# Performance work log

Hardware: AMD Instinct MI355X
Metric: run time of the kernel (lower is better)

Reference implementation:

```python
import jax, jax.numpy as jnp
import numpy as np


def setup_inputs() -> dict:
    key = jax.random.key(0)
    k_x, k_w1, k_w2 = jax.random.split(key, 3)
    B, N, F, H = 32, 1024, 512, 2048
    x = jax.random.normal(k_x, (B, N, F), dtype=jnp.float32)
    # first: orthogonal-ish init (Gaussian is fine as a stand-in for correctness testing)
    W1 = jax.random.normal(k_w1, (H, F), dtype=jnp.float32) / np.sqrt(F)
    b1 = jnp.zeros((H,), dtype=jnp.float32)
    # second: normal(std=0.01)
    W2 = jax.random.normal(k_w2, (F, H), dtype=jnp.float32) * 0.01
    b2 = jnp.zeros((F,), dtype=jnp.float32)
    return {"x": x, "W1": W1, "b1": b1, "W2": W2, "b2": b2, "dim": 1}


def reference(x, W1, b1, W2, b2, dim):
    # Move the target feature axis (1 + dim) to last position.
    x = jnp.moveaxis(x, 1 + dim, -1)  # [B, N, F]
    srt = jnp.argsort(x, axis=-1)     # argsort indices
    inv = jnp.argsort(srt, axis=-1)   # inverse permutation
    # torch: x.scatter(-1, argsort, x) -> out[argsort[i]] = x[i] == gather by inverse
    xs = jnp.take_along_axis(x, inv, axis=-1)
    # 2-layer MLP with skip
    h = jax.nn.relu(jnp.einsum('bnf,hf->bnh', xs, W1) + b1)
    y = jnp.einsum('bnh,fh->bnf', h, W2) + b2 + xs
    # torch: y.scatter(-1, inverse, y) -> out[inverse[i]] = y[i] == gather by argsort
    out = jnp.take_along_axis(y, srt, axis=-1)
    return jnp.moveaxis(out, -1, 1 + dim)
```

## Files before the change

### kernel.cpp

```cpp
#include <hip/hip_runtime.h>
#include <hip/hip_bf16.h>

typedef __hip_bfloat16 bf16;
typedef __attribute__((ext_vector_type(8))) short bf16x8;
typedef __attribute__((ext_vector_type(4))) float f32x4;

#define ASYNC_CP16(gsrc, ldst)                                                              \
  __builtin_amdgcn_global_load_lds(                                                         \
      (const __attribute__((address_space(1))) unsigned int*)(gsrc),                        \
      (__attribute__((address_space(3))) unsigned int*)(ldst), 16, 0, 0)

#define BB 32
#define NN 1024
#define FF 512
#define HH 2048
#define M_ROWS (BB * NN)

__global__ __launch_bounds__(256) void cvt_f32_bf16(const float* __restrict__ s,
                                                    bf16* __restrict__ d, int n) {
  int i = blockIdx.x * 256 + threadIdx.x;
  if (i < n) d[i] = __float2bfloat16(s[i]);
}

__global__ __launch_bounds__(256) void sort_rows_wave(const float* __restrict__ x,
                                                      unsigned* __restrict__ xs_pack,
                                                      unsigned* __restrict__ srt_pack) {
  __shared__ __align__(16) unsigned short scatx[4 * FF];
  const int t = threadIdx.x;
  const int lane = t & 63;
  const int w = t >> 6;
  const size_t row = (size_t)blockIdx.x * 4 + w;
  const float* xr = x + row * FF;

  float4 v0 = *(const float4*)(xr + lane * 8);
  float4 v1 = *(const float4*)(xr + lane * 8 + 4);
  float vals[8] = {v0.x, v0.y, v0.z, v0.w, v1.x, v1.y, v1.z, v1.w};

  unsigned long long key[8];
#pragma unroll
  for (int r = 0; r < 8; r++) {
    unsigned u = __float_as_uint(vals[r]);
    unsigned s = u ^ ((unsigned)((int)u >> 31) | 0x80000000u);
    key[r] = ((unsigned long long)s << 32) | (unsigned)(lane * 8 + r);
  }

#pragma unroll
  for (int k = 2; k <= 512; k <<= 1) {
#pragma unroll
    for (int j = k >> 1; j > 0; j >>= 1) {
      if (j >= 8) {
        const int d = j >> 3;
#pragma unroll
        for (int r = 0; r < 8; r++) {
          unsigned long long o = __shfl_xor(key[r], d, 64);
          bool asc = (((lane * 8 + r) & k) == 0);
          bool lower = ((lane & d) == 0);
          bool keepmin = (asc == lower);
          bool minemin = key[r] < o;
          key[r] = (minemin == keepmin) ? key[r] : o;
        }
      } else {
#pragma unroll
        for (int r = 0; r < 8; r++) {
          if ((r & j) == 0) {
            const int a = r, b = r | j;
            bool asc = (((lane * 8 + a) & k) == 0);
            unsigned long long ka = key[a], kb = key[b];
            bool sw = ((ka > kb) == asc);
            key[a] = sw ? kb : ka;
            key[b] = sw ? ka : kb;
          }
        }
      }
    }
  }

  const int base = w * FF;
  unsigned j8[8];
#pragma unroll
  for (int r = 0; r < 8; r++) {
    j8[r] = (unsigned)key[r] & 0xFFFFu;
    __hip_bfloat16 hb = __float2bfloat16(vals[r]);
    scatx[base + j8[r]] = *(unsigned short*)&hb;
  }

  uint4 so;
  so.x = j8[0] | (j8[1] << 16);
  so.y = j8[2] | (j8[3] << 16);
  so.z = j8[4] | (j8[5] << 16);
  so.w = j8[6] | (j8[7] << 16);
  *(uint4*)(srt_pack + row * 256 + lane * 4) = so;

  __syncthreads();
  uint4 xo = *(const uint4*)&scatx[base + lane * 8];
  *(uint4*)(xs_pack + row * 256 + lane * 4) = xo;
}

template <int RELU, int K, int N>
__global__ __launch_bounds__(512, 4) void gemm_fat(const bf16* __restrict__ A,
                                                   const bf16* __restrict__ Bw,
                                                   const float* __restrict__ bias,
                                                   bf16* __restrict__ C) {
  __shared__ __align__(16) bf16 As[128 * 32];
  __shared__ __align__(16) bf16 Bs[256 * 32];
  const int t = threadIdx.x;
  const int lane = t & 63, wave = t >> 6;
  const int waveM = wave >> 2, waveN = wave & 3;
  const int srow = lane >> 2;
  const int scol = (lane & 3) * 8;
  const size_t mBase = (size_t)blockIdx.x * 128;
  const size_t nBase = (size_t)blockIdx.y * 256;
  const bf16* Ag  = A  + (mBase + wave * 16 + srow) * (size_t)K + scol;
  const bf16* Bg0 = Bw + (nBase + wave * 32 + srow) * (size_t)K + scol;
  const bf16* Bg1 = Bw + (nBase + wave * 32 + 16 + srow) * (size_t)K + scol;
  bf16* Al  = &As[wave * 16 * 32];
  bf16* Bl0 = &Bs[wave * 32 * 32];
  bf16* Bl1 = &Bs[(wave * 32 + 16) * 32];
  const int fr = lane & 15;
  const int fk = (lane >> 4) * 8;

  f32x4 acc[4][4];
  f32x4 zero = {0.f, 0.f, 0.f, 0.f};
#pragma unroll
  for (int i = 0; i < 4; i++)
#pragma unroll
    for (int j = 0; j < 4; j++) acc[i][j] = zero;

  for (int k0 = 0; k0 < K; k0 += 32) {
    ASYNC_CP16(Ag + k0, Al);
    ASYNC_CP16(Bg0 + k0, Bl0);
    ASYNC_CP16(Bg1 + k0, Bl1);
    __syncthreads();
    bf16x8 af[4], bfr[4];
#pragma unroll
    for (int mt = 0; mt < 4; mt++)
      af[mt] = *(const bf16x8*)&As[(waveM * 64 + mt * 16 + fr) * 32 + fk];
#pragma unroll
    for (int nt = 0; nt < 4; nt++)
      bfr[nt] = *(const bf16x8*)&Bs[(waveN * 64 + nt * 16 + fr) * 32 + fk];
#pragma unroll
    for (int mt = 0; mt < 4; mt++)
#pragma unroll
      for (int nt = 0; nt < 4; nt++)
        acc[mt][nt] = __builtin_amdgcn_mfma_f32_16x16x32_bf16(af[mt], bfr[nt], acc[mt][nt], 0, 0, 0);
    __syncthreads();
  }

  const int cn = lane & 15;
  const int cm = (lane >> 4) * 4;
  float b4[4];
#pragma unroll
  for (int nt = 0; nt < 4; nt++) b4[nt] = bias[nBase + waveN * 64 + nt * 16 + cn];
#pragma unroll
  for (int mt = 0; mt < 4; mt++) {
#pragma unroll
    for (int nt = 0; nt < 4; nt++) {
      size_t gn = nBase + waveN * 64 + nt * 16 + cn;
#pragma unroll
      for (int r = 0; r < 4; r++) {
        size_t gm = mBase + waveM * 64 + mt * 16 + cm + r;
        float v = acc[mt][nt][r] + b4[nt];
        if (RELU) v = fmaxf(v, 0.f);
        C[gm * N + gn] = __float2bfloat16(v);
      }
    }
  }
}

__global__ __launch_bounds__(256) void permute_add(const bf16* __restrict__ z,
                                                   const unsigned* __restrict__ srt_pack,
                                                   const float* __restrict__ x,
                                                   float* __restrict__ out) {
  __shared__ __align__(16) unsigned short zr[4][FF];
  const int t = threadIdx.x;
  const int lane = t & 63;
  const int w = t >> 6;
  const size_t row = (size_t)blockIdx.x * 4 + w;

  *(uint4*)&zr[w][lane * 8] = *(const uint4*)(z + row * FF + lane * 8);
  uint4 sv = *(const uint4*)(srt_pack + row * 256 + lane * 4);
  float4 x0 = *(const float4*)(x + row * FF + lane * 8);
  float4 x1 = *(const float4*)(x + row * FF + lane * 8 + 4);
  __syncthreads();

  unsigned idx[8] = {sv.x & 0xFFFFu, sv.x >> 16, sv.y & 0xFFFFu, sv.y >> 16,
                     sv.z & 0xFFFFu, sv.z >> 16, sv.w & 0xFFFFu, sv.w >> 16};
  float xv[8] = {x0.x, x0.y, x0.z, x0.w, x1.x, x1.y, x1.z, x1.w};
  float4 o0, o1;
  float* op = &o0.x;
#pragma unroll
  for (int r = 0; r < 8; r++) {
    float zf = __uint_as_float(((unsigned)zr[w][idx[r]]) << 16);
    ((r < 4) ? (&o0.x) : (&o1.x))[r & 3] = zf + xv[r];
  }
  (void)op;
  *(float4*)(out + row * FF + lane * 8) = o0;
  *(float4*)(out + row * FF + lane * 8 + 4) = o1;
}

extern "C" void kernel_launch(void* const* d_in, const int* in_sizes, int n_in,
                              void* d_out, int out_size, void* d_ws, size_t ws_size,
                              hipStream_t stream) {
  const float* x  = (const float*)d_in[0];
  const float* W1 = (const float*)d_in[1];
  const float* b1 = (const float*)d_in[2];
  const float* W2 = (const float*)d_in[3];
  const float* b2 = (const float*)d_in[4];
  float* out = (float*)d_out;

  char* ws = (char*)d_ws;
  unsigned* xs  = (unsigned*)(ws);
  bf16*     z   = (bf16*)(ws);
  unsigned* srt = (unsigned*)(ws + 33554432);
  bf16* h   = (bf16*)(ws + 67108864);
  bf16* W1b = (bf16*)(ws + 201326592);
  bf16* W2b = (bf16*)(ws + 203423744);

  cvt_f32_bf16<<<(HH * FF + 255) / 256, 256, 0, stream>>>(W1, W1b, HH * FF);
  cvt_f32_bf16<<<(FF * HH + 255) / 256, 256, 0, stream>>>(W2, W2b, FF * HH);
  sort_rows_wave<<<M_ROWS / 4, 256, 0, stream>>>(x, xs, srt);
  gemm_fat<1, FF, HH><<<dim3(M_ROWS / 128, HH / 256), 512, 0, stream>>>((const bf16*)xs, W1b, b1, h);
  gemm_fat<0, HH, FF><<<dim3(M_ROWS / 128, FF / 256), 512, 0, stream>>>(h, W2b, b2, z);
  permute_add<<<M_ROWS / 4, 256, 0, stream>>>(z, srt, x, out);
}
```

Measured before the change: 414.1 us.

## Fuse skip add into second GEMM epilogue, use DPP in sort, merge weight casts

The residual add of the sorted input moves into the second GEMM's epilogue, which reads the bf16 sorted activations. The final permute kernel becomes a pure gather and no longer reads the fp32 input. The bitonic sort replaces some cross-lane shuffles (xor 1, 2, 8) with DPP moves, and the two weight-conversion kernels become one launch. In exchange, the skip term is now bf16-rounded rather than exact fp32, and the epilogue does extra strided bf16 loads.

```diff
diff --git a/kernel.cpp b/kernel.cpp
--- a/kernel.cpp
+++ b/kernel.cpp
@@ -16,10 +16,23 @@
 #define HH 2048
 #define M_ROWS (BB * NN)
 
-__global__ __launch_bounds__(256) void cvt_f32_bf16(const float* __restrict__ s,
-                                                    bf16* __restrict__ d, int n) {
+__global__ __launch_bounds__(256) void cvt_pair(const float* __restrict__ a, bf16* __restrict__ da,
+                                                const float* __restrict__ b, bf16* __restrict__ db,
+                                                int n) {
   int i = blockIdx.x * 256 + threadIdx.x;
-  if (i < n) d[i] = __float2bfloat16(s[i]);
+  if (i < n) {
+    da[i] = __float2bfloat16(a[i]);
+    db[i] = __float2bfloat16(b[i]);
+  }
+}
+
+template <int CTRL>
+__device__ __forceinline__ unsigned long long dpp_xor64(unsigned long long k) {
+  int lo = (int)(unsigned)k;
+  int hi = (int)(unsigned)(k >> 32);
+  int plo = __builtin_amdgcn_update_dpp(lo, lo, CTRL, 0xF, 0xF, false);
+  int phi = __builtin_amdgcn_update_dpp(hi, hi, CTRL, 0xF, 0xF, false);
+  return (((unsigned long long)(unsigned)phi) << 32) | (unsigned)plo;
 }
 
 __global__ __launch_bounds__(256) void sort_rows_wave(const float* __restrict__ x,
@@ -52,7 +65,11 @@
         const int d = j >> 3;
 #pragma unroll
         for (int r = 0; r < 8; r++) {
-          unsigned long long o = __shfl_xor(key[r], d, 64);
+          unsigned long long o;
+          if (d == 1)       o = dpp_xor64<0xB1>(key[r]);
+          else if (d == 2)  o = dpp_xor64<0x4E>(key[r]);
+          else if (d == 8)  o = dpp_xor64<0x128>(key[r]);
+          else              o = __shfl_xor(key[r], d, 64);
           bool asc = (((lane * 8 + r) & k) == 0);
           bool lower = ((lane & d) == 0);
           bool keepmin = (asc == lower);
@@ -96,10 +113,11 @@
   *(uint4*)(xs_pack + row * 256 + lane * 4) = xo;
 }
 
-template <int RELU, int K, int N>
+template <int RELU, int ADDX, int K, int N>
 __global__ __launch_bounds__(512, 4) void gemm_fat(const bf16* __restrict__ A,
                                                    const bf16* __restrict__ Bw,
                                                    const float* __restrict__ bias,
+                                                   const bf16* __restrict__ xs_add,
                                                    bf16* __restrict__ C) {
   __shared__ __align__(16) bf16 As[128 * 32];
   __shared__ __align__(16) bf16 Bs[256 * 32];
@@ -161,39 +179,34 @@
         size_t gm = mBase + waveM * 64 + mt * 16 + cm + r;
         float v = acc[mt][nt][r] + b4[nt];
         if (RELU) v = fmaxf(v, 0.f);
+        if (ADDX) v += __bfloat162float(xs_add[gm * N + gn]);
         C[gm * N + gn] = __float2bfloat16(v);
       }
     }
   }
 }
 
-__global__ __launch_bounds__(256) void permute_add(const bf16* __restrict__ z,
-                                                   const unsigned* __restrict__ srt_pack,
-                                                   const float* __restrict__ x,
-                                                   float* __restrict__ out) {
+__global__ __launch_bounds__(256) void permute_gather(const bf16* __restrict__ zp,
+                                                      const unsigned* __restrict__ srt_pack,
+                                                      float* __restrict__ out) {
   __shared__ __align__(16) unsigned short zr[4][FF];
   const int t = threadIdx.x;
   const int lane = t & 63;
   const int w = t >> 6;
   const size_t row = (size_t)blockIdx.x * 4 + w;
 
-  *(uint4*)&zr[w][lane * 8] = *(const uint4*)(z + row * FF + lane * 8);
+  *(uint4*)&zr[w][lane * 8] = *(const uint4*)(zp + row * FF + lane * 8);
   uint4 sv = *(const uint4*)(srt_pack + row * 256 + lane * 4);
-  float4 x0 = *(const float4*)(x + row * FF + lane * 8);
-  float4 x1 = *(const float4*)(x + row * FF + lane * 8 + 4);
   __syncthreads();
 
   unsigned idx[8] = {sv.x & 0xFFFFu, sv.x >> 16, sv.y & 0xFFFFu, sv.y >> 16,
                      sv.z & 0xFFFFu, sv.z >> 16, sv.w & 0xFFFFu, sv.w >> 16};
-  float xv[8] = {x0.x, x0.y, x0.z, x0.w, x1.x, x1.y, x1.z, x1.w};
   float4 o0, o1;
-  float* op = &o0.x;
 #pragma unroll
   for (int r = 0; r < 8; r++) {
     float zf = __uint_as_float(((unsigned)zr[w][idx[r]]) << 16);
-    ((r < 4) ? (&o0.x) : (&o1.x))[r & 3] = zf + xv[r];
-  }
-  (void)op;
+    ((r < 4) ? (&o0.x) : (&o1.x))[r & 3] = zf;
+  }
   *(float4*)(out + row * FF + lane * 8) = o0;
   *(float4*)(out + row * FF + lane * 8 + 4) = o1;
 }
@@ -210,16 +223,16 @@
 
   char* ws = (char*)d_ws;
   unsigned* xs  = (unsigned*)(ws);
+  bf16*     xsb = (bf16*)(ws);
   bf16*     z   = (bf16*)(ws);
   unsigned* srt = (unsigned*)(ws + 33554432);
   bf16* h   = (bf16*)(ws + 67108864);
   bf16* W1b = (bf16*)(ws + 201326592);
   bf16* W2b = (bf16*)(ws + 203423744);
 
-  cvt_f32_bf16<<<(HH * FF + 255) / 256, 256, 0, stream>>>(W1, W1b, HH * FF);
-  cvt_f32_bf16<<<(FF * HH + 255) / 256, 256, 0, stream>>>(W2, W2b, FF * HH);
+  cvt_pair<<<(HH * FF + 255) / 256, 256, 0, stream>>>(W1, W1b, W2, W2b, HH * FF);
   sort_rows_wave<<<M_ROWS / 4, 256, 0, stream>>>(x, xs, srt);
-  gemm_fat<1, FF, HH><<<dim3(M_ROWS / 128, HH / 256), 512, 0, stream>>>((const bf16*)xs, W1b, b1, h);
-  gemm_fat<0, HH, FF><<<dim3(M_ROWS / 128, FF / 256), 512, 0, stream>>>(h, W2b, b2, z);
-  permute_add<<<M_ROWS / 4, 256, 0, stream>>>(z, srt, x, out);
-}
+  gemm_fat<1, 0, FF, HH><<<dim3(M_ROWS / 128, HH / 256), 512, 0, stream>>>(xsb, W1b, b1, nullptr, h);
+  gemm_fat<0, 1, HH, FF><<<dim3(M_ROWS / 128, FF / 256), 512, 0, stream>>>(h, W2b, b2, xsb, z);
+  permute_gather<<<M_ROWS / 4, 256, 0, stream>>>(z, srt, out);
+}
```

Result: faster. 364.1 us (-12.1%).
